# Kernel optimization log

Measured on AMD Instinct MI355X. Metric: run time of the kernel, lower is better.

The kernel has to match this reference:

```python
import jax, jax.numpy as jnp
import numpy as np

OUT_H = OUT_W = 7          # cfg.output_size
S = 2                      # fixed samples per bin (static replacement for data-dependent ceil(stride))
G = OUT_H * S              # sampling grid side = 14
SCALES = (0.25, 0.125, 0.0625, 0.03125)   # cfg.pooler_scales for P2..P5
SIZES = (256, 128, 64, 32)                # per-level feature H=W


def _roi_align(feat_p2, feat_p3, feat_p4, feat_p5, proposals):
    # Pad all levels to the largest spatial size and stack -> [4, C, 256, 256].
    # Index clamping below never reads past each level's valid region.
    Hmax = SIZES[0]
    levels = []
    for f, s in zip((feat_p2, feat_p3, feat_p4, feat_p5), SIZES):
        levels.append(jnp.pad(f[0], ((0, 0), (0, Hmax - s), (0, Hmax - s))))
    F = jnp.stack(levels)                      # [4, C, 256, 256]

    N = proposals.shape[0]
    pw = proposals[:, 2] - proposals[:, 0]
    ph = proposals[:, 3] - proposals[:, 1]
    # FPN level assignment: floor(2 + log2(sqrt(area)/224)), clamped to [0,3]
    lvl = jnp.clip(jnp.floor(2.0 + jnp.log2(jnp.sqrt(pw * ph) / 224.0)), 0, 3).astype(jnp.int32)

    sc = jnp.asarray(SCALES, proposals.dtype)[lvl]          # [N]
    box = proposals * sc[:, None]                           # scale to feature coords
    bx1, by1, bx2, by2 = box[:, 0], box[:, 1], box[:, 2], box[:, 3]

    w_stride = (bx2 - bx1) / OUT_W
    h_stride = (by2 - by1) / OUT_H
    w_unit = w_stride / S
    h_unit = h_stride / S

    idx = jnp.arange(G, dtype=proposals.dtype) + 0.5        # sample centers
    xs = bx1[:, None] + idx[None, :] * w_unit[:, None]      # [N, G]
    ys = by1[:, None] + idx[None, :] * h_unit[:, None]      # [N, G]
    x = jnp.broadcast_to(xs[:, None, :], (N, G, G))         # [N, Gy, Gx]
    y = jnp.broadcast_to(ys[:, :, None], (N, G, G))

    # Per-level valid extent for clamping (mirrors feature.shape clamps)
    size_l = jnp.asarray(SIZES, jnp.int32)[lvl][:, None, None]   # [N,1,1]

    x0 = jnp.clip(jnp.floor(x).astype(jnp.int32), 0, size_l - 1)
    x1i = jnp.clip(jnp.floor(x).astype(jnp.int32) + 1, 0, size_l - 1)
    y0 = jnp.clip(jnp.floor(y).astype(jnp.int32), 0, size_l - 1)
    y1i = jnp.clip(jnp.floor(y).astype(jnp.int32) + 1, 0, size_l - 1)

    # Weights use the CLAMPED indices, matching the in-place clamp_ in the original.
    x0f, x1f = x0.astype(x.dtype), x1i.astype(x.dtype)
    y0f, y1f = y0.astype(y.dtype), y1i.astype(y.dtype)
    wa = (x1f - x) * (y1f - y)
    wb = (x1f - x) * (y - y0f)
    wc = (x - x0f) * (y1f - y)
    wd = (x - x0f) * (y - y0f)

    lv = jnp.broadcast_to(lvl[:, None, None], (N, G, G))
    la = F[lv, :, y0, x0]      # [N, G, G, C] gathers (irregular access hotspot)
    lb = F[lv, :, y1i, x0]
    lc = F[lv, :, y0, x1i]
    ld = F[lv, :, y1i, x1i]

    interp = (wa[..., None] * la + wb[..., None] * lb
              + wc[..., None] * lc + wd[..., None] * ld)   # [N, G, G, C]

    C = F.shape[1]
    # Adaptive max pool (7,7): exact SxS blocks since G = 7*S
    pooled = interp.reshape(N, OUT_H, S, OUT_W, S, C).max(axis=(2, 4))  # [N,7,7,C]
    return jnp.transpose(pooled, (0, 3, 1, 2))                          # [N,C,7,7]


def setup_inputs() -> dict:
    key = jax.random.key(0)
    k0, k1, k2, k3, k4 = jax.random.split(key, 5)
    C = 256
    feat_p2 = jax.random.normal(k0, (1, C, 256, 256), jnp.float32)
    feat_p3 = jax.random.normal(k1, (1, C, 128, 128), jnp.float32)
    feat_p4 = jax.random.normal(k2, (1, C, 64, 64), jnp.float32)
    feat_p5 = jax.random.normal(k3, (1, C, 32, 32), jnp.float32)
    N = 512
    u = jax.random.uniform(k4, (N, 4), jnp.float32)
    x1 = u[:, 0] * 700.0
    y1 = u[:, 1] * 700.0
    w = 32.0 + u[:, 2] * 292.0
    h = 32.0 + u[:, 3] * 292.0
    proposals = jnp.stack([x1, y1, x1 + w, y1 + h], axis=1)  # [N,4] image coords
    return {"feat_p2": feat_p2, "feat_p3": feat_p3, "feat_p4": feat_p4,
            "feat_p5": feat_p5, "proposals": proposals}


def reference(feat_p2, feat_p3, feat_p4, feat_p5, proposals):
    return _roi_align(feat_p2, feat_p3, feat_p4, feat_p5, proposals)
```

## Files before the change

kernel.cpp:

```cpp
#include <hip/hip_runtime.h>
#include <hip/hip_bf16.h>
#include <math.h>

#define C_CH 256

__global__ __launch_bounds__(256) void transpose_all(
    const float* __restrict__ f0, const float* __restrict__ f1,
    const float* __restrict__ f2, const float* __restrict__ f3,
    __hip_bfloat16* __restrict__ tf) {
  __shared__ float tile[64][65];
  const int b = blockIdx.x;
  const float* src;
  int S, lg;
  size_t dstoff;
  int sb;
  if (b < 4096) {
    src = f0; S = 65536; lg = 10; dstoff = 0;     sb = b;
  } else if (b < 5120) {
    src = f1; S = 16384; lg = 8;  dstoff = 65536; sb = b - 4096;
  } else if (b < 5376) {
    src = f2; S = 4096;  lg = 6;  dstoff = 81920; sb = b - 5120;
  } else {
    src = f3; S = 1024;  lg = 4;  dstoff = 86016; sb = b - 5376;
  }
  const int nsp_m1 = (1 << lg) - 1;
  const int s0 = (sb & nsp_m1) * 64;
  const int c0 = (sb >> lg) * 64;

  const int t = threadIdx.x;
  {
    const int cl = t >> 4;
    const int sp4 = (t & 15) * 4;
    #pragma unroll
    for (int j = 0; j < 4; ++j) {
      const int c = cl + 16 * j;
      const float4 v = *(const float4*)(src + (size_t)(c0 + c) * S + s0 + sp4);
      tile[c][sp4 + 0] = v.x;
      tile[c][sp4 + 1] = v.y;
      tile[c][sp4 + 2] = v.z;
      tile[c][sp4 + 3] = v.w;
    }
  }
  __syncthreads();
  {
    const int spl = t >> 4;
    const int c4 = (t & 15) * 4;
    __hip_bfloat16* dst = tf + (dstoff + (size_t)s0) * C_CH + c0;
    #pragma unroll
    for (int j = 0; j < 4; ++j) {
      const int sp = spl + 16 * j;
      union { ushort4 u; __hip_bfloat16 h[4]; } p;
      p.h[0] = __float2bfloat16(tile[c4 + 0][sp]);
      p.h[1] = __float2bfloat16(tile[c4 + 1][sp]);
      p.h[2] = __float2bfloat16(tile[c4 + 2][sp]);
      p.h[3] = __float2bfloat16(tile[c4 + 3][sp]);
      *(ushort4*)(dst + (size_t)sp * C_CH + c4) = p.u;
    }
  }
}

__device__ __forceinline__ float bfu(unsigned short s) {
  union { unsigned u; float f; } v;
  v.u = (unsigned)s << 16;
  return v.f;
}

#define OPAD 260

__global__ __launch_bounds__(512) void roi_bf16(
    const unsigned short* __restrict__ tf,
    const float* __restrict__ proposals, float* __restrict__ out) {
  __shared__ int xo0[14], xo1[14], yo0[14], yo1[14];
  __shared__ float wxa[14], wxb[14], wya[14], wyb[14];
  __shared__ float obuf[49 * OPAD];

  const int n = blockIdx.x;
  const int t = threadIdx.x;
  const int lane = t & 63;
  const int w = t >> 6;

  const float px1 = proposals[n * 4 + 0];
  const float py1 = proposals[n * 4 + 1];
  const float px2 = proposals[n * 4 + 2];
  const float py2 = proposals[n * 4 + 3];
  float lt = 2.0f + log2f(sqrtf((px2 - px1) * (py2 - py1)) / 224.0f);
  int lvl = (int)floorf(lt);
  lvl = lvl < 0 ? 0 : (lvl > 3 ? 3 : lvl);

  const float scales[4] = {0.25f, 0.125f, 0.0625f, 0.03125f};
  const int sizes[4] = {256, 128, 64, 32};
  const int offs[4] = {0, 65536, 81920, 86016};
  const float sc = scales[lvl];
  const int sz = sizes[lvl];

  const float bx1 = px1 * sc, by1 = py1 * sc;
  const float w_unit = ((px2 - px1) * sc / 7.0f) * 0.5f;
  const float h_unit = ((py2 - py1) * sc / 7.0f) * 0.5f;

  if (t < 14) {
    const int i = t;
    float x = bx1 + ((float)i + 0.5f) * w_unit;
    int xf = (int)floorf(x);
    int x0 = min(max(xf, 0), sz - 1);
    int x1 = min(max(xf + 1, 0), sz - 1);
    wxa[i] = (float)x1 - x;
    wxb[i] = x - (float)x0;
    xo0[i] = x0 * C_CH;
    xo1[i] = x1 * C_CH;
  } else if (t >= 64 && t < 78) {
    const int i = t - 64;
    float y = by1 + ((float)i + 0.5f) * h_unit;
    int yf = (int)floorf(y);
    int y0 = min(max(yf, 0), sz - 1);
    int y1 = min(max(yf + 1, 0), sz - 1);
    wya[i] = (float)y1 - y;
    wyb[i] = y - (float)y0;
    yo0[i] = y0 * sz * C_CH;
    yo1[i] = y1 * sz * C_CH;
  }
  __syncthreads();

  if (w < 7) {
    const int oh = w;
    const int gy0 = 2 * oh, gy1 = 2 * oh + 1;
    const unsigned short* base = tf + (size_t)offs[lvl] * C_CH + lane * 4;
    const unsigned short* r00 = base + yo0[gy0];
    const unsigned short* r01 = base + yo1[gy0];
    const unsigned short* r10 = base + yo0[gy1];
    const unsigned short* r11 = base + yo1[gy1];
    const float wy0a = wya[gy0], wy0b = wyb[gy0];
    const float wy1a = wya[gy1], wy1b = wyb[gy1];

    float mm[7][4];
    #pragma unroll
    for (int j = 0; j < 7; ++j)
      #pragma unroll
      for (int k = 0; k < 4; ++k) mm[j][k] = -INFINITY;

    #pragma unroll
    for (int gx = 0; gx < 14; ++gx) {
      const int xa = xo0[gx], xb = xo1[gx];
      const ushort4 A0 = *(const ushort4*)(r00 + xa);
      const ushort4 A1 = *(const ushort4*)(r00 + xb);
      const ushort4 B0 = *(const ushort4*)(r01 + xa);
      const ushort4 B1 = *(const ushort4*)(r01 + xb);
      const ushort4 C0 = *(const ushort4*)(r10 + xa);
      const ushort4 C1 = *(const ushort4*)(r10 + xb);
      const ushort4 D0 = *(const ushort4*)(r11 + xa);
      const ushort4 D1 = *(const ushort4*)(r11 + xb);
      const float fa = wxa[gx], fb = wxb[gx];
      const int j = gx >> 1;
      const unsigned short* a0 = (const unsigned short*)&A0;
      const unsigned short* a1 = (const unsigned short*)&A1;
      const unsigned short* b0 = (const unsigned short*)&B0;
      const unsigned short* b1 = (const unsigned short*)&B1;
      const unsigned short* c0 = (const unsigned short*)&C0;
      const unsigned short* c1 = (const unsigned short*)&C1;
      const unsigned short* d0 = (const unsigned short*)&D0;
      const unsigned short* d1 = (const unsigned short*)&D1;
      #pragma unroll
      for (int k = 0; k < 4; ++k) {
        const float h00 = fa * bfu(a0[k]) + fb * bfu(a1[k]);
        const float h01 = fa * bfu(b0[k]) + fb * bfu(b1[k]);
        const float va = wy0a * h00 + wy0b * h01;
        const float h10 = fa * bfu(c0[k]) + fb * bfu(c1[k]);
        const float h11 = fa * bfu(d0[k]) + fb * bfu(d1[k]);
        const float vb = wy1a * h10 + wy1b * h11;
        mm[j][k] = fmaxf(mm[j][k], fmaxf(va, vb));
      }
    }

    #pragma unroll
    for (int ow = 0; ow < 7; ++ow) {
      float4 v = make_float4(mm[ow][0], mm[ow][1], mm[ow][2], mm[ow][3]);
      *(float4*)&obuf[(oh * 7 + ow) * OPAD + lane * 4] = v;
    }
  }
  __syncthreads();

  float* ob = out + (size_t)n * (C_CH * 49);
  for (int i = t; i < C_CH * 49; i += 512) {
    const unsigned c = (unsigned)i / 49u;
    const unsigned p = (unsigned)i - c * 49u;
    ob[i] = obuf[p * OPAD + c];
  }
}

__global__ __launch_bounds__(64) void roi_fallback(
    const float* __restrict__ f0, const float* __restrict__ f1,
    const float* __restrict__ f2, const float* __restrict__ f3,
    const float* __restrict__ proposals, float* __restrict__ out) {
  __shared__ int xo0[14], xo1[14], yo0[14], yo1[14];
  __shared__ float wxa[14], wxb[14], wya[14], wyb[14];
  const int n = blockIdx.x;
  const int cblk = blockIdx.y;
  const int lane = threadIdx.x;
  const int c = cblk * 64 + lane;
  const float px1 = proposals[n * 4 + 0];
  const float py1 = proposals[n * 4 + 1];
  const float px2 = proposals[n * 4 + 2];
  const float py2 = proposals[n * 4 + 3];
  float lt = 2.0f + log2f(sqrtf((px2 - px1) * (py2 - py1)) / 224.0f);
  int lvl = (int)floorf(lt);
  lvl = lvl < 0 ? 0 : (lvl > 3 ? 3 : lvl);
  const float scales[4] = {0.25f, 0.125f, 0.0625f, 0.03125f};
  const int sizes[4] = {256, 128, 64, 32};
  const float sc = scales[lvl];
  const int sz = sizes[lvl];
  const float bx1 = px1 * sc, by1 = py1 * sc;
  const float w_unit = ((px2 - px1) * sc / 7.0f) * 0.5f;
  const float h_unit = ((py2 - py1) * sc / 7.0f) * 0.5f;
  if (lane < 14) {
    float x = bx1 + ((float)lane + 0.5f) * w_unit;
    int xf = (int)floorf(x);
    int x0 = min(max(xf, 0), sz - 1);
    int x1 = min(max(xf + 1, 0), sz - 1);
    wxa[lane] = (float)x1 - x;
    wxb[lane] = x - (float)x0;
    xo0[lane] = x0;
    xo1[lane] = x1;
  } else if (lane >= 32 && lane < 46) {
    const int i = lane - 32;
    float y = by1 + ((float)i + 0.5f) * h_unit;
    int yf = (int)floorf(y);
    int y0 = min(max(yf, 0), sz - 1);
    int y1 = min(max(yf + 1, 0), sz - 1);
    wya[i] = (float)y1 - y;
    wyb[i] = y - (float)y0;
    yo0[i] = y0 * sz;
    yo1[i] = y1 * sz;
  }
  __syncthreads();
  const float* fl = (lvl == 0) ? f0 : (lvl == 1) ? f1 : (lvl == 2) ? f2 : f3;
  const float* base = fl + (size_t)c * sz * sz;
  for (int oh = 0; oh < 7; ++oh) {
    float mm[7];
    #pragma unroll
    for (int ow = 0; ow < 7; ++ow) mm[ow] = -INFINITY;
    #pragma unroll
    for (int sy = 0; sy < 2; ++sy) {
      const int gy = oh * 2 + sy;
      const float* r0 = base + yo0[gy];
      const float* r1 = base + yo1[gy];
      const float wy0 = wya[gy], wy1 = wyb[gy];
      #pragma unroll
      for (int gx = 0; gx < 14; ++gx) {
        float v = wy0 * (wxa[gx] * r0[xo0[gx]] + wxb[gx] * r0[xo1[gx]]) +
                  wy1 * (wxa[gx] * r1[xo0[gx]] + wxb[gx] * r1[xo1[gx]]);
        mm[gx >> 1] = fmaxf(mm[gx >> 1], v);
      }
    }
    #pragma unroll
    for (int ow = 0; ow < 7; ++ow)
      out[((size_t)n * C_CH + c) * 49 + oh * 7 + ow] = mm[ow];
  }
}

extern "C" void kernel_launch(void* const* d_in, const int* in_sizes, int n_in,
                              void* d_out, int out_size, void* d_ws,
                              size_t ws_size, hipStream_t stream) {
  const float* f0 = (const float*)d_in[0];
  const float* f1 = (const float*)d_in[1];
  const float* f2 = (const float*)d_in[2];
  const float* f3 = (const float*)d_in[3];
  const float* props = (const float*)d_in[4];
  float* out = (float*)d_out;
  const int N = in_sizes[4] / 4;

  const size_t needed = (size_t)87040 * C_CH * sizeof(__hip_bfloat16);
  if (ws_size >= needed) {
    __hip_bfloat16* tf = (__hip_bfloat16*)d_ws;
    transpose_all<<<5440, 256, 0, stream>>>(f0, f1, f2, f3, tf);
    roi_bf16<<<N, 512, 0, stream>>>((const unsigned short*)tf, props, out);
  } else {
    roi_fallback<<<dim3(N, 4), 64, 0, stream>>>(f0, f1, f2, f3, props, out);
  }
}
```

Measured before the change: 144.9 us.

## Transpose full 256-channel tiles with XOR-swizzled LDS and float4 reads

The fp32-to-bf16 NHWC transpose now processes all 256 channels for 64 spatial positions per block, with 512 threads and 1360 blocks instead of 64x64 tiles in 5440 blocks. Shared memory uses an XOR swizzle so each thread can read a float4 of four consecutive channels, and each row writes a full 512-byte channel line. The aim is fewer LDS accesses and bank conflicts plus contiguous output rows. In exchange it needs 64KB of LDS per block, which limits occupancy to roughly one or two blocks per CU.

```diff
diff --git a/kernel.cpp b/kernel.cpp
--- a/kernel.cpp
+++ b/kernel.cpp
@@ -4,57 +4,61 @@
 
 #define C_CH 256
 
-__global__ __launch_bounds__(256) void transpose_all(
+__global__ __launch_bounds__(512) void transpose_all(
     const float* __restrict__ f0, const float* __restrict__ f1,
     const float* __restrict__ f2, const float* __restrict__ f3,
     __hip_bfloat16* __restrict__ tf) {
-  __shared__ float tile[64][65];
+  __shared__ float tile[64 * 256];
   const int b = blockIdx.x;
   const float* src;
-  int S, lg;
+  int S;
   size_t dstoff;
   int sb;
-  if (b < 4096) {
-    src = f0; S = 65536; lg = 10; dstoff = 0;     sb = b;
-  } else if (b < 5120) {
-    src = f1; S = 16384; lg = 8;  dstoff = 65536; sb = b - 4096;
-  } else if (b < 5376) {
-    src = f2; S = 4096;  lg = 6;  dstoff = 81920; sb = b - 5120;
+  if (b < 1024) {
+    src = f0; S = 65536; dstoff = 0;     sb = b;
+  } else if (b < 1280) {
+    src = f1; S = 16384; dstoff = 65536; sb = b - 1024;
+  } else if (b < 1344) {
+    src = f2; S = 4096;  dstoff = 81920; sb = b - 1280;
   } else {
-    src = f3; S = 1024;  lg = 4;  dstoff = 86016; sb = b - 5376;
-  }
-  const int nsp_m1 = (1 << lg) - 1;
-  const int s0 = (sb & nsp_m1) * 64;
-  const int c0 = (sb >> lg) * 64;
+    src = f3; S = 1024;  dstoff = 86016; sb = b - 1344;
+  }
+  const int s0 = sb * 64;
 
   const int t = threadIdx.x;
   {
-    const int cl = t >> 4;
     const int sp4 = (t & 15) * 4;
-    #pragma unroll
-    for (int j = 0; j < 4; ++j) {
-      const int c = cl + 16 * j;
-      const float4 v = *(const float4*)(src + (size_t)(c0 + c) * S + s0 + sp4);
-      tile[c][sp4 + 0] = v.x;
-      tile[c][sp4 + 1] = v.y;
-      tile[c][sp4 + 2] = v.z;
-      tile[c][sp4 + 3] = v.w;
+    const int cb = t >> 4;
+    const int K = t & 15;
+    #pragma unroll
+    for (int j = 0; j < 8; ++j) {
+      const int c = cb + 32 * j;
+      const float4 v = *(const float4*)(src + (size_t)c * S + s0 + sp4);
+      const int q = (c >> 2) ^ K;
+      const int r = c & 3;
+      float* p = &tile[sp4 * 256 + q * 4 + r];
+      p[0 * 256] = v.x;
+      p[1 * 256] = v.y;
+      p[2 * 256] = v.z;
+      p[3 * 256] = v.w;
     }
   }
   __syncthreads();
   {
-    const int spl = t >> 4;
-    const int c4 = (t & 15) * 4;
-    __hip_bfloat16* dst = tf + (dstoff + (size_t)s0) * C_CH + c0;
-    #pragma unroll
-    for (int j = 0; j < 4; ++j) {
-      const int sp = spl + 16 * j;
+    const int lane = t & 63;
+    const int w = t >> 6;
+    __hip_bfloat16* dst = tf + (dstoff + (size_t)s0) * C_CH;
+    #pragma unroll
+    for (int j = 0; j < 8; ++j) {
+      const int sp = w + 8 * j;
+      const int K = (sp >> 2) & 15;
+      const float4 v = *(const float4*)&tile[sp * 256 + ((lane ^ K) * 4)];
       union { ushort4 u; __hip_bfloat16 h[4]; } p;
-      p.h[0] = __float2bfloat16(tile[c4 + 0][sp]);
-      p.h[1] = __float2bfloat16(tile[c4 + 1][sp]);
-      p.h[2] = __float2bfloat16(tile[c4 + 2][sp]);
-      p.h[3] = __float2bfloat16(tile[c4 + 3][sp]);
-      *(ushort4*)(dst + (size_t)sp * C_CH + c4) = p.u;
+      p.h[0] = __float2bfloat16(v.x);
+      p.h[1] = __float2bfloat16(v.y);
+      p.h[2] = __float2bfloat16(v.z);
+      p.h[3] = __float2bfloat16(v.w);
+      *(ushort4*)(dst + (size_t)sp * C_CH + lane * 4) = p.u;
     }
   }
 }
@@ -270,7 +274,7 @@
   const size_t needed = (size_t)87040 * C_CH * sizeof(__hip_bfloat16);
   if (ws_size >= needed) {
     __hip_bfloat16* tf = (__hip_bfloat16*)d_ws;
-    transpose_all<<<5440, 256, 0, stream>>>(f0, f1, f2, f3, tf);
+    transpose_all<<<1360, 512, 0, stream>>>(f0, f1, f2, f3, tf);
     roi_bf16<<<N, 512, 0, stream>>>((const unsigned short*)tf, props, out);
   } else {
     roi_fallback<<<dim3(N, 4), 64, 0, stream>>>(f0, f1, f2, f3, props, out);
```

After: 148.6 us. 1.03x slower.

## Fuse transpose and ROI pooling into one persistent cooperative kernel with grid sync

Applied to the files above, without the earlier changes.

Replaces the two launches (layout transpose to bf16, then ROI align) with a single persistent cooperative kernel of 512 blocks. Each block loops over transpose tiles with double-buffered shared memory, prefetching the next tile while storing the current one. After a grid-wide barrier the same blocks loop over the proposals. This removes one launch and the gap between kernels, at the cost of a grid sync and a persistent grid that may underfill or oversubscribe CUs. A standard two-kernel fallback runs if the cooperative launch fails.

```diff
diff --git a/kernel.cpp b/kernel.cpp
--- a/kernel.cpp
+++ b/kernel.cpp
@@ -1,8 +1,220 @@
 #include <hip/hip_runtime.h>
 #include <hip/hip_bf16.h>
+#include <hip/hip_cooperative_groups.h>
 #include <math.h>
 
+namespace cg = cooperative_groups;
+
 #define C_CH 256
+#define OPAD 260
+#define NTILES 5440
+#define FGRID 512
+
+__device__ __forceinline__ float bfu(unsigned short s) {
+  union { unsigned u; float f; } v;
+  v.u = (unsigned)s << 16;
+  return v.f;
+}
+
+struct TInfo { const float* src; size_t dstbase; int S; };
+
+__device__ __forceinline__ TInfo tinfo(int b, const float* f0, const float* f1,
+                                       const float* f2, const float* f3) {
+  TInfo ti; int lg; size_t dstoff; int sb;
+  if (b < 4096)      { ti.src = f0; ti.S = 65536; lg = 10; dstoff = 0;     sb = b; }
+  else if (b < 5120) { ti.src = f1; ti.S = 16384; lg = 8;  dstoff = 65536; sb = b - 4096; }
+  else if (b < 5376) { ti.src = f2; ti.S = 4096;  lg = 6;  dstoff = 81920; sb = b - 5120; }
+  else               { ti.src = f3; ti.S = 1024;  lg = 4;  dstoff = 86016; sb = b - 5376; }
+  const int nsp_m1 = (1 << lg) - 1;
+  const int s0 = (sb & nsp_m1) * 64;
+  const int c0 = (sb >> lg) * 64;
+  ti.src += (size_t)c0 * ti.S + s0;
+  ti.dstbase = (dstoff + (size_t)s0) * C_CH + c0;
+  return ti;
+}
+
+__device__ __forceinline__ void t_load(const TInfo& ti, float (*tile)[65],
+                                       int cl, int sp4) {
+  #pragma unroll
+  for (int j = 0; j < 2; ++j) {
+    const int c = cl + 32 * j;
+    const float4 v = *(const float4*)(ti.src + (size_t)c * ti.S + sp4);
+    tile[c][sp4 + 0] = v.x;
+    tile[c][sp4 + 1] = v.y;
+    tile[c][sp4 + 2] = v.z;
+    tile[c][sp4 + 3] = v.w;
+  }
+}
+
+__device__ __forceinline__ void t_store(const TInfo& ti,
+                                        unsigned short* __restrict__ tf,
+                                        const float (*tile)[65], int spl,
+                                        int c4) {
+  #pragma unroll
+  for (int j = 0; j < 2; ++j) {
+    const int sp = spl + 32 * j;
+    union { ushort4 u; __hip_bfloat16 h[4]; } p;
+    p.h[0] = __float2bfloat16(tile[c4 + 0][sp]);
+    p.h[1] = __float2bfloat16(tile[c4 + 1][sp]);
+    p.h[2] = __float2bfloat16(tile[c4 + 2][sp]);
+    p.h[3] = __float2bfloat16(tile[c4 + 3][sp]);
+    *(ushort4*)(tf + ti.dstbase + (size_t)sp * C_CH + c4) = p.u;
+  }
+}
+
+__global__ __launch_bounds__(512, 4) void fused_all(
+    const float* __restrict__ f0, const float* __restrict__ f1,
+    const float* __restrict__ f2, const float* __restrict__ f3,
+    const float* __restrict__ proposals, unsigned short* __restrict__ tf,
+    float* __restrict__ out, int N) {
+  __shared__ union {
+    float tile[2][64][65];
+    float obuf[49 * OPAD];
+  } sm;
+  __shared__ int xo0[14], xo1[14], yo0[14], yo1[14];
+  __shared__ float wxa[14], wxb[14], wya[14], wyb[14];
+
+  const int t = threadIdx.x;
+
+  {
+    const int cl = t >> 4;
+    const int sp4 = (t & 15) * 4;
+    const int spl = t >> 4;
+    const int c4 = (t & 15) * 4;
+
+    int b = blockIdx.x;
+    TInfo ti = tinfo(b, f0, f1, f2, f3);
+    t_load(ti, sm.tile[0], cl, sp4);
+    int cur = 0;
+    for (;;) {
+      const int bn = b + FGRID;
+      const bool more = (bn < NTILES);
+      TInfo tin;
+      if (more) tin = tinfo(bn, f0, f1, f2, f3);
+      __syncthreads();
+      if (more) t_load(tin, sm.tile[cur ^ 1], cl, sp4);
+      t_store(ti, tf, sm.tile[cur], spl, c4);
+      if (!more) break;
+      ti = tin;
+      b = bn;
+      cur ^= 1;
+    }
+  }
+
+  cg::this_grid().sync();
+
+  for (int n = blockIdx.x; n < N; n += FGRID) {
+    const int lane = t & 63;
+    const int w = t >> 6;
+
+    const float px1 = proposals[n * 4 + 0];
+    const float py1 = proposals[n * 4 + 1];
+    const float px2 = proposals[n * 4 + 2];
+    const float py2 = proposals[n * 4 + 3];
+    float lt = 2.0f + log2f(sqrtf((px2 - px1) * (py2 - py1)) / 224.0f);
+    int lvl = (int)floorf(lt);
+    lvl = lvl < 0 ? 0 : (lvl > 3 ? 3 : lvl);
+
+    const float scales[4] = {0.25f, 0.125f, 0.0625f, 0.03125f};
+    const int sizes[4] = {256, 128, 64, 32};
+    const int offs[4] = {0, 65536, 81920, 86016};
+    const float sc = scales[lvl];
+    const int sz = sizes[lvl];
+
+    const float bx1 = px1 * sc, by1 = py1 * sc;
+    const float w_unit = ((px2 - px1) * sc / 7.0f) * 0.5f;
+    const float h_unit = ((py2 - py1) * sc / 7.0f) * 0.5f;
+
+    if (t < 14) {
+      const int i = t;
+      float x = bx1 + ((float)i + 0.5f) * w_unit;
+      int xf = (int)floorf(x);
+      int x0 = min(max(xf, 0), sz - 1);
+      int x1 = min(max(xf + 1, 0), sz - 1);
+      wxa[i] = (float)x1 - x;
+      wxb[i] = x - (float)x0;
+      xo0[i] = x0 * C_CH;
+      xo1[i] = x1 * C_CH;
+    } else if (t >= 64 && t < 78) {
+      const int i = t - 64;
+      float y = by1 + ((float)i + 0.5f) * h_unit;
+      int yf = (int)floorf(y);
+      int y0 = min(max(yf, 0), sz - 1);
+      int y1 = min(max(yf + 1, 0), sz - 1);
+      wya[i] = (float)y1 - y;
+      wyb[i] = y - (float)y0;
+      yo0[i] = y0 * sz * C_CH;
+      yo1[i] = y1 * sz * C_CH;
+    }
+    __syncthreads();
+
+    if (w < 7) {
+      const int oh = w;
+      const int gy0 = 2 * oh, gy1 = 2 * oh + 1;
+      const unsigned short* base = tf + (size_t)offs[lvl] * C_CH + lane * 4;
+      const unsigned short* r00 = base + yo0[gy0];
+      const unsigned short* r01 = base + yo1[gy0];
+      const unsigned short* r10 = base + yo0[gy1];
+      const unsigned short* r11 = base + yo1[gy1];
+      const float wy0a = wya[gy0], wy0b = wyb[gy0];
+      const float wy1a = wya[gy1], wy1b = wyb[gy1];
+
+      float mm[7][4];
+      #pragma unroll
+      for (int j = 0; j < 7; ++j)
+        #pragma unroll
+        for (int k = 0; k < 4; ++k) mm[j][k] = -INFINITY;
+
+      #pragma unroll
+      for (int gx = 0; gx < 14; ++gx) {
+        const int xa = xo0[gx], xb = xo1[gx];
+        const ushort4 A0 = *(const ushort4*)(r00 + xa);
+        const ushort4 A1 = *(const ushort4*)(r00 + xb);
+        const ushort4 B0 = *(const ushort4*)(r01 + xa);
+        const ushort4 B1 = *(const ushort4*)(r01 + xb);
+        const ushort4 C0 = *(const ushort4*)(r10 + xa);
+        const ushort4 C1 = *(const ushort4*)(r10 + xb);
+        const ushort4 D0 = *(const ushort4*)(r11 + xa);
+        const ushort4 D1 = *(const ushort4*)(r11 + xb);
+        const float fa = wxa[gx], fb = wxb[gx];
+        const int j = gx >> 1;
+        const unsigned short* a0 = (const unsigned short*)&A0;
+        const unsigned short* a1 = (const unsigned short*)&A1;
+        const unsigned short* b0 = (const unsigned short*)&B0;
+        const unsigned short* b1 = (const unsigned short*)&B1;
+        const unsigned short* c0 = (const unsigned short*)&C0;
+        const unsigned short* c1 = (const unsigned short*)&C1;
+        const unsigned short* d0 = (const unsigned short*)&D0;
+        const unsigned short* d1 = (const unsigned short*)&D1;
+        #pragma unroll
+        for (int k = 0; k < 4; ++k) {
+          const float h00 = fa * bfu(a0[k]) + fb * bfu(a1[k]);
+          const float h01 = fa * bfu(b0[k]) + fb * bfu(b1[k]);
+          const float va = wy0a * h00 + wy0b * h01;
+          const float h10 = fa * bfu(c0[k]) + fb * bfu(c1[k]);
+          const float h11 = fa * bfu(d0[k]) + fb * bfu(d1[k]);
+          const float vb = wy1a * h10 + wy1b * h11;
+          mm[j][k] = fmaxf(mm[j][k], fmaxf(va, vb));
+        }
+      }
+
+      #pragma unroll
+      for (int ow = 0; ow < 7; ++ow) {
+        float4 v = make_float4(mm[ow][0], mm[ow][1], mm[ow][2], mm[ow][3]);
+        *(float4*)&sm.obuf[(oh * 7 + ow) * OPAD + lane * 4] = v;
+      }
+    }
+    __syncthreads();
+
+    float* ob = out + (size_t)n * (C_CH * 49);
+    for (int i = t; i < C_CH * 49; i += 512) {
+      const unsigned c = (unsigned)i / 49u;
+      const unsigned p = (unsigned)i - c * 49u;
+      ob[i] = sm.obuf[p * OPAD + c];
+    }
+    __syncthreads();
+  }
+}
 
 __global__ __launch_bounds__(256) void transpose_all(
     const float* __restrict__ f0, const float* __restrict__ f1,
@@ -58,14 +270,6 @@
     }
   }
 }
-
-__device__ __forceinline__ float bfu(unsigned short s) {
-  union { unsigned u; float f; } v;
-  v.u = (unsigned)s << 16;
-  return v.f;
-}
-
-#define OPAD 260
 
 __global__ __launch_bounds__(512) void roi_bf16(
     const unsigned short* __restrict__ tf,
@@ -265,13 +469,28 @@
   const float* f3 = (const float*)d_in[3];
   const float* props = (const float*)d_in[4];
   float* out = (float*)d_out;
-  const int N = in_sizes[4] / 4;
+  int N = in_sizes[4] / 4;
 
   const size_t needed = (size_t)87040 * C_CH * sizeof(__hip_bfloat16);
   if (ws_size >= needed) {
-    __hip_bfloat16* tf = (__hip_bfloat16*)d_ws;
-    transpose_all<<<5440, 256, 0, stream>>>(f0, f1, f2, f3, tf);
-    roi_bf16<<<N, 512, 0, stream>>>((const unsigned short*)tf, props, out);
+    unsigned short* tf = (unsigned short*)d_ws;
+    void* args[8];
+    args[0] = (void*)&f0;
+    args[1] = (void*)&f1;
+    args[2] = (void*)&f2;
+    args[3] = (void*)&f3;
+    args[4] = (void*)&props;
+    args[5] = (void*)&tf;
+    args[6] = (void*)&out;
+    args[7] = (void*)&N;
+    hipError_t err = hipLaunchCooperativeKernel(
+        reinterpret_cast<const void*>(fused_all), dim3(FGRID), dim3(512), args,
+        0, stream);
+    if (err != hipSuccess) {
+      transpose_all<<<5440, 256, 0, stream>>>(f0, f1, f2, f3,
+                                              (__hip_bfloat16*)d_ws);
+      roi_bf16<<<N, 512, 0, stream>>>(tf, props, out);
+    }
   } else {
     roi_fallback<<<dim3(N, 4), 64, 0, stream>>>(f0, f1, f2, f3, props, out);
   }
```

Result: slower. 228.8 us (+58.0%).

## Software-prefetch next gather column and XOR-swizzle shared output buffer

Applied to the files above, without the earlier changes.

The bilinear gather loop now issues the eight loads for the next sampling column before computing the current one, a manual double-buffering meant to hide global-load latency. Separately, the padded shared-memory output buffer is replaced by an unpadded buffer with an XOR swizzle on float4 groups. This keeps bank conflicts low in the transposed read-out while using less LDS. The prefetch raises register pressure in an already unrolled loop, and the compiler may already have been scheduling these loads early.

```diff
diff --git a/kernel.cpp b/kernel.cpp
--- a/kernel.cpp
+++ b/kernel.cpp
@@ -65,14 +65,12 @@
   return v.f;
 }
 
-#define OPAD 260
-
 __global__ __launch_bounds__(512) void roi_bf16(
     const unsigned short* __restrict__ tf,
     const float* __restrict__ proposals, float* __restrict__ out) {
   __shared__ int xo0[14], xo1[14], yo0[14], yo1[14];
   __shared__ float wxa[14], wxb[14], wya[14], wyb[14];
-  __shared__ float obuf[49 * OPAD];
+  __shared__ float obuf[49 * 256];
 
   const int n = blockIdx.x;
   const int t = threadIdx.x;
@@ -137,17 +135,33 @@
       #pragma unroll
       for (int k = 0; k < 4; ++k) mm[j][k] = -INFINITY;
 
+    ushort4 nA0, nA1, nB0, nB1, nC0, nC1, nD0, nD1;
+    {
+      const int xa = xo0[0], xb = xo1[0];
+      nA0 = *(const ushort4*)(r00 + xa);
+      nA1 = *(const ushort4*)(r00 + xb);
+      nB0 = *(const ushort4*)(r01 + xa);
+      nB1 = *(const ushort4*)(r01 + xb);
+      nC0 = *(const ushort4*)(r10 + xa);
+      nC1 = *(const ushort4*)(r10 + xb);
+      nD0 = *(const ushort4*)(r11 + xa);
+      nD1 = *(const ushort4*)(r11 + xb);
+    }
     #pragma unroll
     for (int gx = 0; gx < 14; ++gx) {
-      const int xa = xo0[gx], xb = xo1[gx];
-      const ushort4 A0 = *(const ushort4*)(r00 + xa);
-      const ushort4 A1 = *(const ushort4*)(r00 + xb);
-      const ushort4 B0 = *(const ushort4*)(r01 + xa);
-      const ushort4 B1 = *(const ushort4*)(r01 + xb);
-      const ushort4 C0 = *(const ushort4*)(r10 + xa);
-      const ushort4 C1 = *(const ushort4*)(r10 + xb);
-      const ushort4 D0 = *(const ushort4*)(r11 + xa);
-      const ushort4 D1 = *(const ushort4*)(r11 + xb);
+      const ushort4 A0 = nA0, A1 = nA1, B0 = nB0, B1 = nB1;
+      const ushort4 C0 = nC0, C1 = nC1, D0 = nD0, D1 = nD1;
+      if (gx < 13) {
+        const int xa = xo0[gx + 1], xb = xo1[gx + 1];
+        nA0 = *(const ushort4*)(r00 + xa);
+        nA1 = *(const ushort4*)(r00 + xb);
+        nB0 = *(const ushort4*)(r01 + xa);
+        nB1 = *(const ushort4*)(r01 + xb);
+        nC0 = *(const ushort4*)(r10 + xa);
+        nC1 = *(const ushort4*)(r10 + xb);
+        nD0 = *(const ushort4*)(r11 + xa);
+        nD1 = *(const ushort4*)(r11 + xb);
+      }
       const float fa = wxa[gx], fb = wxb[gx];
       const int j = gx >> 1;
       const unsigned short* a0 = (const unsigned short*)&A0;
@@ -172,8 +186,9 @@
 
     #pragma unroll
     for (int ow = 0; ow < 7; ++ow) {
+      const int p = oh * 7 + ow;
       float4 v = make_float4(mm[ow][0], mm[ow][1], mm[ow][2], mm[ow][3]);
-      *(float4*)&obuf[(oh * 7 + ow) * OPAD + lane * 4] = v;
+      *(float4*)&obuf[p * 256 + ((lane ^ p) & 63) * 4] = v;
     }
   }
   __syncthreads();
@@ -182,7 +197,8 @@
   for (int i = t; i < C_CH * 49; i += 512) {
     const unsigned c = (unsigned)i / 49u;
     const unsigned p = (unsigned)i - c * 49u;
-    ob[i] = obuf[p * OPAD + c];
+    const unsigned q = ((c >> 2) ^ p) & 63u;
+    ob[i] = obuf[p * 256 + q * 4 + (c & 3)];
   }
 }
 
```

New measurement: 146.7 us. No clear change (+1.3%).
